# Performance work log

Hardware: AMD Instinct MI355X
Metric: run time of the kernel (lower is better)

The kernel has to match this reference:

```python
import jax, jax.numpy as jnp
import numpy as np

B, N_C, N_T = 8, 2048, 2048
D_S, D_F = 2, 1
K = 32
EMB_OBS = 4
H = 64
N_RBF = 16
NUM_BLKS = 6
RBF_GAMMA = 10.0


def _layer_norm(x, g, b):
    m = jnp.mean(x, -1, keepdims=True)
    v = jnp.var(x, -1, keepdims=True)
    return (x - m) * jax.lax.rsqrt(v + 1e-6) * g + b


def setup_inputs() -> dict:
    key = jax.random.key(0)
    ks = jax.random.split(key, 16)
    D_IN = EMB_OBS + D_S + D_F  # obs-flag embed + coords + features = 7
    return {
        "s_ctx": jax.random.normal(ks[0], (B, N_C, D_S)),
        "f_ctx": jax.random.normal(ks[1], (B, N_C, D_F)),
        "s_test": jax.random.normal(ks[2], (B, N_T, D_S)),
        "obs_table": jax.random.normal(ks[3], (2, EMB_OBS)) * 0.1,
        "emb_w0": jax.random.normal(ks[4], (D_IN, 256)) / np.sqrt(D_IN),
        "emb_b0": jnp.zeros((256,)),
        "emb_w1": jax.random.normal(ks[5], (256, 128)) / np.sqrt(256.0),
        "emb_b1": jnp.zeros((128,)),
        "emb_w2": jax.random.normal(ks[6], (128, H)) / np.sqrt(128.0),
        "emb_b2": jnp.zeros((H,)),
        "ln_g": jnp.ones((H,)),
        "ln_b": jnp.zeros((H,)),
        "rbf_centers": jnp.tile(jnp.linspace(0.0, 4.0, N_RBF)[None, :], (NUM_BLKS, 1)),
        "rbf_w": jax.random.normal(ks[7], (NUM_BLKS, N_RBF)) / np.sqrt(N_RBF),
        "rbf_b": jnp.zeros((NUM_BLKS,)),
        "blk_w1": jax.random.normal(ks[8], (NUM_BLKS, 2 * H, 2 * H)) / np.sqrt(2.0 * H),
        "blk_b1": jnp.zeros((NUM_BLKS, 2 * H)),
        "blk_w2": jax.random.normal(ks[9], (NUM_BLKS, 2 * H, H)) / np.sqrt(2.0 * H),
        "blk_b2": jnp.zeros((NUM_BLKS, H)),
        "blk_ln_g": jnp.ones((NUM_BLKS, H)),
        "blk_ln_b": jnp.zeros((NUM_BLKS, H)),
        "head_w0": jax.random.normal(ks[10], (H, 256)) / np.sqrt(float(H)),
        "head_b0": jnp.zeros((256,)),
        "head_w1": jax.random.normal(ks[11], (256, 64)) / np.sqrt(256.0),
        "head_b1": jnp.zeros((64,)),
        "head_w2": jax.random.normal(ks[12], (64, 2)) / np.sqrt(64.0),
        "head_b2": jnp.zeros((2,)),
    }


def reference(s_ctx, f_ctx, s_test, obs_table, emb_w0, emb_b0, emb_w1, emb_b1,
              emb_w2, emb_b2, ln_g, ln_b, rbf_centers, rbf_w, rbf_b,
              blk_w1, blk_b1, blk_w2, blk_b2, blk_ln_g, blk_ln_b,
              head_w0, head_b0, head_w1, head_b1, head_w2, head_b2):
    Bq, N_c = s_ctx.shape[:2]
    N_t = s_test.shape[1]

    # --- embed: obs flag + coords + (zeroed for test) function values ---
    obs_c = jnp.broadcast_to(obs_table[1], (Bq, N_c, EMB_OBS))  # observed = 1
    obs_t = jnp.broadcast_to(obs_table[0], (Bq, N_t, EMB_OBS))  # unobserved = 0
    f_test = jnp.zeros((Bq, N_t, f_ctx.shape[-1]), f_ctx.dtype)
    ctx = jnp.concatenate([obs_c, s_ctx, f_ctx], -1)
    test = jnp.concatenate([obs_t, s_test, f_test], -1)

    def emb(x):
        h = jax.nn.gelu(x @ emb_w0 + emb_b0)
        h = jax.nn.gelu(h @ emb_w1 + emb_b1)
        return h @ emb_w2 + emb_b2

    x_ctx = _layer_norm(emb(ctx), ln_g, ln_b)
    x_test = _layer_norm(emb(test), ln_g, ln_b)

    # --- kNN graph build (queries -> context senders) ---
    def knn(q, s):
        d2 = jnp.sum((q[:, :, None, :] - s[:, None, :, :]) ** 2, -1)  # (B, Nq, Nc)
        neg, idx = jax.lax.top_k(-d2, K)
        return idx, jnp.sqrt(jnp.maximum(-neg, 1e-12))

    idx_cc, d_cc = knn(s_ctx, s_ctx)
    idx_ct, d_ct = knn(s_test, s_ctx)
    off = (jnp.arange(Bq) * N_c)[:, None, None]
    senders = jnp.concatenate([(idx_cc + off).reshape(-1), (idx_ct + off).reshape(-1)])
    edges = jnp.concatenate([d_cc.reshape(-1), d_ct.reshape(-1)])
    nodes = jnp.concatenate([x_ctx.reshape(Bq * N_c, H), x_test.reshape(Bq * N_t, H)], 0)
    n_node = Bq * (N_c + N_t)
    # receivers = repeat(arange(n_node), K): each node owns a contiguous K-edge block
    send2d = senders.reshape(n_node, K)
    e2d = edges.reshape(n_node, K)
    mask2d = jnp.isfinite(e2d)
    e_safe = jnp.where(mask2d, e2d, 0.0)

    # --- RBF-biased message-passing blocks ---
    for l in range(NUM_BLKS):
        feats = jnp.exp(-RBF_GAMMA * (e_safe[..., None] - rbf_centers[l]) ** 2)  # (n_node, K, N_RBF)
        bias = feats @ rbf_w[l] + rbf_b[l]                                       # (n_node, K)
        bias = jnp.where(mask2d, bias, -1e9)
        w = jax.nn.softmax(bias, axis=-1)
        agg = jnp.einsum('nk,nkh->nh', w, nodes[send2d])  # gather senders + weighted sum
        h = jnp.concatenate([nodes, agg], -1)
        h = jax.nn.gelu(h @ blk_w1[l] + blk_b1[l])
        h = h @ blk_w2[l] + blk_b2[l]
        nodes = _layer_norm(nodes + h, blk_ln_g[l], blk_ln_b[l])

    # --- head + diagonal MVN ---
    x_t = nodes[-Bq * N_t:].reshape(Bq, N_t, H)
    h = jax.nn.gelu(x_t @ head_w0 + head_b0)
    h = jax.nn.gelu(h @ head_w1 + head_b1)
    out = h @ head_w2 + head_b2
    mean = out[..., 0]
    std = jax.nn.softplus(out[..., 1]) + 1e-3
    return mean, std
```

## Files before the change

kernel.cpp:

```cpp
#include <hip/hip_runtime.h>
#include <hip/hip_bf16.h>
#include <hip/hip_fp16.h>
#include <math.h>

using bf16 = __hip_bfloat16;

#define N_CTX   2048
#define N_TST   2048
#define NB      8
#define KNN     32
#define HDIM    64
#define NRBF    16
#define N_CTX_NODES (NB * N_CTX)
#define N_NODE      (NB * (N_CTX + N_TST))
#define POOL_CAP 256

typedef __attribute__((ext_vector_type(8))) short short8;
typedef __attribute__((ext_vector_type(4))) float f32x4;

#define SWZ(r, k) ((k) ^ (((r) & 7) << 3))

__device__ __forceinline__ bool is_f32(const void* probe) {
    return ((const unsigned short*)probe)[0] == 0;
}
template<bool F32>
__device__ __forceinline__ float ldT(const void* p, int i) {
    if constexpr (F32) return ((const float*)p)[i];
    else               return __bfloat162float(((const bf16*)p)[i]);
}
__device__ __forceinline__ float ld(const void* p, int i, bool f32) {
    return f32 ? ((const float*)p)[i]
               : __bfloat162float(((const bf16*)p)[i]);
}
__device__ __forceinline__ unsigned short f2b(float x) {
    bf16 h = __float2bfloat16(x); unsigned short u;
    __builtin_memcpy(&u, &h, 2); return u;
}
__device__ __forceinline__ float b2f(unsigned short u) {
    bf16 h; __builtin_memcpy(&h, &u, 2); return __bfloat162float(h);
}
__device__ __forceinline__ unsigned short f2h(float x) {
    __half h = __float2half(x); unsigned short u;
    __builtin_memcpy(&u, &h, 2); return u;
}
__device__ __forceinline__ float h2f(unsigned short u) {
    __half h; __builtin_memcpy(&h, &u, 2); return __half2float(h);
}
__device__ __forceinline__ float gelu_tanh(float x) {
    float u = -1.5957691216057308f * (x + 0.044715f * x * x * x);
    return x * __builtin_amdgcn_rcpf(1.0f + __expf(u));
}
__device__ __forceinline__ unsigned long long shfl_u64(unsigned long long v, int src) {
    int lo = __shfl((int)(unsigned)v, src);
    int hi = __shfl((int)(unsigned)(v >> 32), src);
    return ((unsigned long long)(unsigned)hi << 32) | (unsigned)lo;
}

__device__ __forceinline__ void batch_barrier(unsigned* cnt, unsigned target) {
    __syncthreads();
    if (threadIdx.x == 0) {
        __hip_atomic_fetch_add(cnt, 1u, __ATOMIC_RELEASE, __HIP_MEMORY_SCOPE_AGENT);
        unsigned v;
        do {
            v = __hip_atomic_load(cnt, __ATOMIC_ACQUIRE, __HIP_MEMORY_SCOPE_AGENT);
            if (v < target) __builtin_amdgcn_s_sleep(2);
        } while (v < target);
    }
    __syncthreads();
}

__global__ void prep_w_kernel(const void* w1, const void* w2, const void* probe,
                              unsigned short* __restrict__ w1t,
                              unsigned short* __restrict__ w2t) {
    bool f32 = is_f32(probe);
    int l = blockIdx.x >> 3, s = blockIdx.x & 7, t = threadIdx.x;
    for (int idx = s * 2048 + t; idx < (s + 1) * 2048; idx += 256) {
        int k = idx >> 7, c = idx & 127;
        w1t[l * 16384 + c * 128 + k] = f2b(ld(w1, l * 16384 + idx, f32));
    }
    for (int idx = s * 1024 + t; idx < (s + 1) * 1024; idx += 256) {
        int k = idx >> 6, c = idx & 63;
        w2t[l * 8192 + c * 128 + k] = f2b(ld(w2, l * 8192 + idx, f32));
    }
}

template<bool F32>
__device__ __forceinline__ void embed_body(
        const void* s_ctx, const void* f_ctx, const void* s_test, const void* obs,
        const void* w0, const void* b0, const void* w1, const void* b1,
        const void* w2, const void* b2, const void* ln_g, const void* ln_b,
        unsigned short* __restrict__ ctxb, float* __restrict__ testf,
        unsigned short* A, unsigned short* W, unsigned short* H0, unsigned short* W2) {
    int tid = threadIdx.x, w = tid >> 6, l = tid & 63;
    int nb = blockIdx.x * 64;
    bool is_test = (nb >= N_CTX_NODES);
    int loc0 = is_test ? nb - N_CTX_NODES : nb;
    int b = loc0 >> 11;

    for (int idx = tid; idx < 64 * 128; idx += 512) A[idx] = 0;
    for (int idx = tid; idx < 256 * 128; idx += 512) W[idx] = 0;
    __syncthreads();

    {   int nn = tid >> 3, slot = tid & 7;
        if (slot < 7) {
            int loc = loc0 + nn;
            int i = loc & (N_CTX - 1);
            float v;
            if (slot < 4)       v = ldT<F32>(obs, (is_test ? 0 : 1) * 4 + slot);
            else if (slot < 6)  v = is_test ? ldT<F32>(s_test, (b * N_TST + i) * 2 + slot - 4)
                                            : ldT<F32>(s_ctx,  (b * N_CTX + i) * 2 + slot - 4);
            else                v = is_test ? 0.0f : ldT<F32>(f_ctx, b * N_CTX + i);
            A[nn * 128 + SWZ(nn, slot)] = f2b(v);
        }
    }
    for (int idx = tid; idx < 7 * 256; idx += 512) {
        int k = idx >> 8, c = idx & 255;
        W[c * 128 + SWZ(c, k)] = f2b(ldT<F32>(w0, idx));
    }
    __syncthreads();

    {
        int rt = w & 3, co = w >> 2;
        int ra = rt * 16 + (l & 15);
        int kb = (l >> 4) << 3;
        short8 av = *(const short8*)&A[ra * 128 + SWZ(ra, kb)];
        f32x4 acc[8];
        #pragma unroll
        for (int c8 = 0; c8 < 8; ++c8) acc[c8] = (f32x4){0.f, 0.f, 0.f, 0.f};
        #pragma unroll
        for (int c8 = 0; c8 < 8; ++c8) {
            int cb = co * 8 + c8;
            int rb = cb * 16 + (l & 15);
            short8 bv = *(const short8*)&W[rb * 128 + SWZ(rb, kb)];
            acc[c8] = __builtin_amdgcn_mfma_f32_16x16x32_bf16(av, bv, acc[c8], 0, 0, 0);
        }
        #pragma unroll
        for (int c8 = 0; c8 < 8; ++c8) {
            int col = (co * 8 + c8) * 16 + (l & 15);
            float bb = ldT<F32>(b0, col);
            #pragma unroll
            for (int reg = 0; reg < 4; ++reg) {
                int r = rt * 16 + (l >> 4) * 4 + reg;
                H0[r * 256 + SWZ(r, col)] = f2b(gelu_tanh(acc[c8][reg] + bb));
            }
        }
    }
    __syncthreads();

    for (int idx = tid; idx < 256 * 128; idx += 512) {
        int k = idx >> 7, c = idx & 127;
        W[c * 256 + SWZ(c, k)] = f2b(ldT<F32>(w1, idx));
    }
    for (int idx = tid; idx < 128 * 64; idx += 512) {
        int k = idx >> 6, c = idx & 63;
        W2[c * 128 + SWZ(c, k)] = f2b(ldT<F32>(w2, idx));
    }
    __syncthreads();

    {
        int rt = w & 3, cq = w >> 2;
        int ra = rt * 16 + (l & 15);
        f32x4 acc[4];
        #pragma unroll
        for (int c4 = 0; c4 < 4; ++c4) acc[c4] = (f32x4){0.f, 0.f, 0.f, 0.f};
        #pragma unroll
        for (int ks = 0; ks < 8; ++ks) {
            int kb = ks * 32 + ((l >> 4) << 3);
            short8 av = *(const short8*)&H0[ra * 256 + SWZ(ra, kb)];
            #pragma unroll
            for (int c4 = 0; c4 < 4; ++c4) {
                int cb = cq * 4 + c4;
                int rb = cb * 16 + (l & 15);
                short8 bv = *(const short8*)&W[rb * 256 + SWZ(rb, kb)];
                acc[c4] = __builtin_amdgcn_mfma_f32_16x16x32_bf16(av, bv, acc[c4], 0, 0, 0);
            }
        }
        #pragma unroll
        for (int c4 = 0; c4 < 4; ++c4) {
            int col = (cq * 4 + c4) * 16 + (l & 15);
            float bb = ldT<F32>(b1, col);
            #pragma unroll
            for (int reg = 0; reg < 4; ++reg) {
                int r = rt * 16 + (l >> 4) * 4 + reg;
                A[r * 128 + SWZ(r, col)] = f2b(gelu_tanh(acc[c4][reg] + bb));
            }
        }
    }
    __syncthreads();

    if (w < 4) {
        f32x4 a2[4];
        #pragma unroll
        for (int cb = 0; cb < 4; ++cb) a2[cb] = (f32x4){0.f, 0.f, 0.f, 0.f};
        int ra = w * 16 + (l & 15);
        #pragma unroll
        for (int ks = 0; ks < 4; ++ks) {
            int kb = ks * 32 + ((l >> 4) << 3);
            short8 av = *(const short8*)&A[ra * 128 + SWZ(ra, kb)];
            #pragma unroll
            for (int cb = 0; cb < 4; ++cb) {
                int rb = cb * 16 + (l & 15);
                short8 bv = *(const short8*)&W2[rb * 128 + SWZ(rb, kb)];
                a2[cb] = __builtin_amdgcn_mfma_f32_16x16x32_bf16(av, bv, a2[cb], 0, 0, 0);
            }
        }
        int colb = l & 15;
        float g4[4], bb4[4], b24[4];
        #pragma unroll
        for (int cb = 0; cb < 4; ++cb) {
            int col = cb * 16 + colb;
            g4[cb]  = ldT<F32>(ln_g, col);
            bb4[cb] = ldT<F32>(ln_b, col);
            b24[cb] = ldT<F32>(b2,  col);
        }
        #pragma unroll
        for (int reg = 0; reg < 4; ++reg) {
            int r = w * 16 + (l >> 4) * 4 + reg;
            float vv[4]; float s = 0.f, s2 = 0.f;
            #pragma unroll
            for (int cb = 0; cb < 4; ++cb) {
                float v = a2[cb][reg] + b24[cb];
                vv[cb] = v; s += v; s2 += v * v;
            }
            #pragma unroll
            for (int o = 8; o > 0; o >>= 1) { s += __shfl_xor(s, o); s2 += __shfl_xor(s2, o); }
            float m = s / 64.0f;
            float var = s2 / 64.0f - m * m;
            float rs = rsqrtf(var + 1e-6f);
            #pragma unroll
            for (int cb = 0; cb < 4; ++cb) {
                int col = cb * 16 + colb;
                float val = (vv[cb] - m) * rs * g4[cb] + bb4[cb];
                if (is_test) testf[(loc0 + r) * HDIM + col] = val;
                else         ctxb[(size_t)(nb + r) * HDIM + col] = f2b(val);
            }
        }
    }
}

__global__ __launch_bounds__(512)
void embed_kernel(const void* s_ctx, const void* f_ctx, const void* s_test,
                  const void* obs, const void* w0, const void* b0,
                  const void* w1, const void* b1, const void* w2, const void* b2,
                  const void* ln_g, const void* ln_b,
                  unsigned short* __restrict__ ctxb, float* __restrict__ testf) {
    __shared__ unsigned short A[64 * 128];
    __shared__ unsigned short W[256 * 128];
    __shared__ unsigned short H0[64 * 256];
    __shared__ unsigned short W2[64 * 128];
    if (is_f32(ln_g))
        embed_body<true>(s_ctx, f_ctx, s_test, obs, w0, b0, w1, b1, w2, b2,
                         ln_g, ln_b, ctxb, testf, A, W, H0, W2);
    else
        embed_body<false>(s_ctx, f_ctx, s_test, obs, w0, b0, w1, b1, w2, b2,
                          ln_g, ln_b, ctxb, testf, A, W, H0, W2);
}

__global__ __launch_bounds__(512) void knn_kernel(const void* s_ctx, const void* s_test,
                                                  const void* probe,
                                                  unsigned short* __restrict__ knn_idx) {
    bool f32 = is_f32(probe);
    int w = threadIdx.x >> 6, l = threadIdx.x & 63;
    int n = blockIdx.x * 8 + w;
    __shared__ float cx[N_CTX], cy[N_CTX];
    __shared__ unsigned long long pool[8][POOL_CAP];
    __shared__ unsigned pcnt[8];

    bool is_test = (n >= N_CTX_NODES);
    int loc = is_test ? n - N_CTX_NODES : n;
    int b = loc >> 11, q = loc & (N_CTX - 1);

    for (int j = threadIdx.x; j < N_CTX; j += 512) {
        cx[j] = ld(s_ctx, (b * N_CTX + j) * 2 + 0, f32);
        cy[j] = ld(s_ctx, (b * N_CTX + j) * 2 + 1, f32);
    }
    __syncthreads();

    float qx = is_test ? ld(s_test, (b * N_TST + q) * 2 + 0, f32) : cx[q];
    float qy = is_test ? ld(s_test, (b * N_TST + q) * 2 + 1, f32) : cy[q];

    unsigned dbits[32];
    unsigned bmin = 0xFFFFFFFFu;
    #pragma unroll
    for (int i = 0; i < 32; ++i) {
        int j = i * 64 + l;
        float dx = qx - cx[j], dy = qy - cy[j];
        float d2 = __fadd_rn(__fmul_rn(dx, dx), __fmul_rn(dy, dy));
        unsigned ub = __float_as_uint(d2);
        dbits[i] = ub;
        bmin = min(bmin, ub);
    }

    unsigned T = 0;
    #pragma unroll
    for (int bit = 31; bit >= 0; --bit) {
        unsigned trial = T | (1u << bit);
        int c = __popcll(__ballot(bmin < trial));
        if (c < 32) T = trial;
    }

    if (l == 0) pcnt[w] = 0;
    unsigned mycnt = 0;
    #pragma unroll
    for (int i = 0; i < 32; ++i) mycnt += (dbits[i] <= T) ? 1u : 0u;
    unsigned off = atomicAdd(&pcnt[w], mycnt);
    #pragma unroll
    for (int i = 0; i < 32; ++i) {
        if (dbits[i] <= T) {
            if (off < POOL_CAP)
                pool[w][off] = ((unsigned long long)dbits[i] << 32) | (unsigned)(i * 64 + l);
            ++off;
        }
    }
    asm volatile("s_waitcnt lgkmcnt(0)" ::: "memory");
    unsigned M = pcnt[w];
    if (M > POOL_CAP) M = POOL_CAP;

    if (M <= 128) {
        unsigned long long my0 = (l < (int)M) ? pool[w][l] : ~0ull;
        unsigned long long my1 = (64 + l < (int)M) ? pool[w][64 + l] : ~0ull;
        unsigned r0 = 0, r1 = 0;
        unsigned M0 = M < 64 ? M : 64;
        for (unsigned jp = 0; jp < M0; ++jp) {
            unsigned long long v = shfl_u64(my0, (int)jp);
            r0 += (v < my0) ? 1u : 0u;
            r1 += (v < my1) ? 1u : 0u;
        }
        for (unsigned jp = 64; jp < M; ++jp) {
            unsigned long long v = shfl_u64(my1, (int)(jp - 64));
            r0 += (v < my0) ? 1u : 0u;
            r1 += (v < my1) ? 1u : 0u;
        }
        if (l < (int)M && r0 < KNN)
            knn_idx[(size_t)n * KNN + r0] = (unsigned short)(my0 & 0xFFFFu);
        if (64 + l < (int)M && r1 < KNN)
            knn_idx[(size_t)n * KNN + r1] = (unsigned short)(my1 & 0xFFFFu);
    } else {
        for (unsigned m = l; m < M; m += 64) {
            unsigned long long me = pool[w][m];
            unsigned rank = 0;
            for (unsigned jp = 0; jp < M; ++jp)
                rank += (pool[w][jp] < me) ? 1u : 0u;
            if (rank < KNN)
                knn_idx[(size_t)n * KNN + rank] = (unsigned short)(me & 0xFFFFu);
        }
    }
}

__global__ __launch_bounds__(1024, 4)
void mp_coop_kernel(unsigned short* __restrict__ ctxA, unsigned short* __restrict__ ctxB,
                    float* __restrict__ testf,
                    const unsigned short* __restrict__ kidx,
                    unsigned* __restrict__ bar,
                    const unsigned short* __restrict__ w1tg,
                    const unsigned short* __restrict__ w2tg,
                    const void* s_ctx, const void* s_test,
                    const void* rbf_c, const void* rbf_w, const void* rbf_b,
                    const void* b1, const void* b2,
                    const void* lng, const void* lnb) {
    bool f32 = is_f32(lng);
    int tid = threadIdx.x, w = tid >> 6, l = tid & 63;

    int batch = blockIdx.x & 7;
    int slot  = blockIdx.x >> 3;
    bool isctx = (slot < 16);
    int lslot = slot & 15;
    int seg0 = batch * N_CTX + lslot * 128;
    int n0   = (isctx ? 0 : N_CTX_NODES) + seg0;
    int bofs = batch * N_CTX;
    unsigned* cnt = bar + batch * 16;

    __shared__ float          state[128 * 64];
    __shared__ unsigned short A0[128 * 128];
    __shared__ unsigned short h1s[128 * 128];
    __shared__ unsigned short wk_l[128 * 32];
    __shared__ unsigned short kidx_l[128 * 32];
    __shared__ unsigned short d_l[128 * 32];

    for (int idx = tid; idx < 128 * 64; idx += 1024)
        state[idx] = isctx ? b2f(ctxA[n0 * 64 + idx]) : testf[seg0 * 64 + idx];

    for (int idx = tid; idx < 4096; idx += 1024) {
        int i = idx >> 5, kk = idx & 31;
        int n = n0 + i;
        int q = lslot * 128 + i;
        float qx = isctx ? ld(s_ctx, (bofs + q) * 2 + 0, f32)
                         : ld(s_test, (batch * N_TST + q) * 2 + 0, f32);
        float qy = isctx ? ld(s_ctx, (bofs + q) * 2 + 1, f32)
                         : ld(s_test, (batch * N_TST + q) * 2 + 1, f32);
        int si = (int)kidx[(size_t)n * KNN + kk];
        kidx_l[idx] = (unsigned short)si;
        float dx = qx - ld(s_ctx, (bofs + si) * 2 + 0, f32);
        float dy = qy - ld(s_ctx, (bofs + si) * 2 + 1, f32);
        float d2 = __fadd_rn(__fmul_rn(dx, dx), __fmul_rn(dy, dy));
        d_l[idx] = f2h(sqrtf(fmaxf(d2, 1e-12f)));
    }
    __syncthreads();

    const unsigned short* cur = ctxA;
    unsigned short* nxt = ctxB;

    for (int layer = 0; layer < 6; ++layer) {
        for (int p = 0; p < 4; ++p) {
            int i = w * 8 + p * 2 + (l >> 5);
            int kk = l & 31;
            float d = h2f(d_l[i * 32 + kk]);
            float bias = ld(rbf_b, layer, f32);
            #pragma unroll
            for (int j = 0; j < NRBF; ++j) {
                float c = ld(rbf_c, layer * NRBF + j, f32);
                float u = d - c;
                bias += expf(-10.0f * u * u) * ld(rbf_w, layer * NRBF + j, f32);
            }
            float m = bias;
            #pragma unroll
            for (int o = 16; o > 0; o >>= 1) m = fmaxf(m, __shfl_xor(m, o));
            float e = expf(bias - m), s = e;
            #pragma unroll
            for (int o = 16; o > 0; o >>= 1) s += __shfl_xor(s, o);
            wk_l[i * 32 + kk] = f2h(e / s);
        }
        {
            int m = l & 31, h = l >> 5;
            for (int i = w * 8; i < w * 8 + 8; ++i) {
                A0[i * 128 + SWZ(i, l)] = f2b(state[i * 64 + l]);
                float a0 = 0.f, a1 = 0.f, c0 = 0.f, c1 = 0.f;
                #pragma unroll
                for (int k = 0; k < 16; k += 2) {
                    {
                        int kk = 2 * k + h;
                        int si = (int)kidx_l[i * 32 + kk];
                        unsigned u = *(const unsigned*)(cur + (size_t)(bofs + si) * 64 + 2 * m);
                        float wkv = h2f(wk_l[i * 32 + kk]);
                        a0 += wkv * __uint_as_float(u << 16);
                        a1 += wkv * __uint_as_float(u & 0xFFFF0000u);
                    }
                    {
                        int kk = 2 * (k + 1) + h;
                        int si = (int)kidx_l[i * 32 + kk];
                        unsigned u = *(const unsigned*)(cur + (size_t)(bofs + si) * 64 + 2 * m);
                        float wkv = h2f(wk_l[i * 32 + kk]);
                        c0 += wkv * __uint_as_float(u << 16);
                        c1 += wkv * __uint_as_float(u & 0xFFFF0000u);
                    }
                }
                a0 += c0; a1 += c1;
                a0 += __shfl_xor(a0, 32);
                a1 += __shfl_xor(a1, 32);
                if (h == 0) {
                    unsigned pk = (unsigned)f2b(a0) | ((unsigned)f2b(a1) << 16);
                    *(unsigned*)&A0[i * 128 + SWZ(i, 64 + 2 * m)] = pk;
                }
            }
        }
        __syncthreads();

        {
            const unsigned short* wB = w1tg + layer * 16384;
            f32x4 acc[4];
            #pragma unroll
            for (int c4 = 0; c4 < 4; ++c4) acc[c4] = (f32x4){0.f, 0.f, 0.f, 0.f};
            int ra = (w & 7) * 16 + (l & 15);
            #pragma unroll
            for (int ks = 0; ks < 4; ++ks) {
                int kb = ks * 32 + ((l >> 4) << 3);
                short8 av = *(const short8*)&A0[ra * 128 + SWZ(ra, kb)];
                #pragma unroll
                for (int c4 = 0; c4 < 4; ++c4) {
                    int cb = (w >> 3) * 4 + c4;
                    int rb = cb * 16 + (l & 15);
                    short8 bv = *(const short8*)&wB[rb * 128 + kb];
                    acc[c4] = __builtin_amdgcn_mfma_f32_16x16x32_bf16(av, bv, acc[c4], 0, 0, 0);
                }
            }
            #pragma unroll
            for (int c4 = 0; c4 < 4; ++c4) {
                int col = ((w >> 3) * 4 + c4) * 16 + (l & 15);
                float bb = ld(b1, layer * 128 + col, f32);
                #pragma unroll
                for (int reg = 0; reg < 4; ++reg) {
                    int r = (w & 7) * 16 + (l >> 4) * 4 + reg;
                    h1s[r * 128 + SWZ(r, col)] = f2b(gelu_tanh(acc[c4][reg] + bb));
                }
            }
        }
        __syncthreads();

        if (w < 8) {
            const unsigned short* wB2 = w2tg + layer * 8192;
            f32x4 a2[4];
            #pragma unroll
            for (int cb = 0; cb < 4; ++cb) a2[cb] = (f32x4){0.f, 0.f, 0.f, 0.f};
            int ra = w * 16 + (l & 15);
            #pragma unroll
            for (int ks = 0; ks < 4; ++ks) {
                int kb = ks * 32 + ((l >> 4) << 3);
                short8 av = *(const short8*)&h1s[ra * 128 + SWZ(ra, kb)];
                #pragma unroll
                for (int cb = 0; cb < 4; ++cb) {
                    int rb = cb * 16 + (l & 15);
                    short8 bv = *(const short8*)&wB2[rb * 128 + kb];
                    a2[cb] = __builtin_amdgcn_mfma_f32_16x16x32_bf16(av, bv, a2[cb], 0, 0, 0);
                }
            }
            int colb = l & 15;
            float g4[4], bb4[4], b24[4];
            #pragma unroll
            for (int cb = 0; cb < 4; ++cb) {
                int col = cb * 16 + colb;
                g4[cb]  = ld(lng, layer * 64 + col, f32);
                bb4[cb] = ld(lnb, layer * 64 + col, f32);
                b24[cb] = ld(b2,  layer * 64 + col, f32);
            }
            #pragma unroll
            for (int reg = 0; reg < 4; ++reg) {
                int r = w * 16 + (l >> 4) * 4 + reg;
                float vv[4]; float s = 0.f, s2 = 0.f;
                #pragma unroll
                for (int cb = 0; cb < 4; ++cb) {
                    int col = cb * 16 + colb;
                    float v = a2[cb][reg] + b24[cb] + state[r * 64 + col];
                    vv[cb] = v; s += v; s2 += v * v;
                }
                #pragma unroll
                for (int o = 8; o > 0; o >>= 1) { s += __shfl_xor(s, o); s2 += __shfl_xor(s2, o); }
                float m = s / 64.0f;
                float var = s2 / 64.0f - m * m;
                float rs = rsqrtf(var + 1e-6f);
                #pragma unroll
                for (int cb = 0; cb < 4; ++cb) {
                    int col = cb * 16 + colb;
                    state[r * 64 + col] = (vv[cb] - m) * rs * g4[cb] + bb4[cb];
                }
            }
        }
        __syncthreads();

        if (layer < 5) {
            if (isctx)
                for (int idx = tid; idx < 128 * 64; idx += 1024)
                    nxt[n0 * 64 + idx] = f2b(state[idx]);
            batch_barrier(cnt, 32u * (unsigned)(layer + 1));
            const unsigned short* t1 = cur; cur = nxt; nxt = (unsigned short*)t1;
        }
    }

    if (!isctx)
        for (int idx = tid; idx < 128 * 64; idx += 1024)
            testf[seg0 * 64 + idx] = state[idx];
}

template<bool F32>
__device__ __forceinline__ void head_body(
        const float* __restrict__ testf, const void* w0, const void* b0,
        const void* w1, const void* b1, const void* w2, const void* b2, void* out,
        float (*xs)[64], float (*h0)[256], float (*h1)[64]) {
    int t = threadIdx.x;
    int pb = blockIdx.x * 16;

    for (int idx = t; idx < 1024; idx += 256)
        xs[idx >> 6][idx & 63] = testf[(pb + (idx >> 6)) * HDIM + (idx & 63)];
    __syncthreads();

    {
        float bb = ldT<F32>(b0, t);
        float a[16];
        #pragma unroll
        for (int j = 0; j < 16; ++j) a[j] = bb;
        for (int i = 0; i < 64; ++i) {
            float wv = ldT<F32>(w0, i * 256 + t);
            #pragma unroll
            for (int j = 0; j < 16; ++j) a[j] += xs[j][i] * wv;
        }
        #pragma unroll
        for (int j = 0; j < 16; ++j) h0[j][t] = gelu_tanh(a[j]);
    }
    __syncthreads();

    {
        int c = t & 63, g = t >> 6;
        float bb = ldT<F32>(b1, c);
        float a0 = bb, a1 = bb, a2 = bb, a3 = bb;
        for (int i = 0; i < 256; ++i) {
            float wv = ldT<F32>(w1, i * 64 + c);
            a0 += h0[g][i] * wv;      a1 += h0[g + 4][i] * wv;
            a2 += h0[g + 8][i] * wv;  a3 += h0[g + 12][i] * wv;
        }
        h1[g][c]      = gelu_tanh(a0); h1[g + 4][c]  = gelu_tanh(a1);
        h1[g + 8][c]  = gelu_tanh(a2); h1[g + 12][c] = gelu_tanh(a3);
    }
    __syncthreads();

    if (t < 32) {
        int nn = t >> 1, j = t & 1;
        float a = ldT<F32>(b2, j);
        for (int i = 0; i < 64; ++i) a += h1[nn][i] * ldT<F32>(w2, i * 2 + j);
        float r;
        if (j == 0) r = a;
        else        r = fmaxf(a, 0.0f) + log1pf(expf(-fabsf(a))) + 1e-3f;
        int oi = j * 16384 + pb + nn;
        if constexpr (F32) ((float*)out)[oi] = r;
        else               ((bf16*)out)[oi]  = __float2bfloat16(r);
    }
}

__global__ void head_kernel(const float* __restrict__ testf,
                            const void* w0, const void* b0, const void* w1, const void* b1,
                            const void* w2, const void* b2, const void* probe, void* out) {
    __shared__ float xs[16][64];
    __shared__ float h0[16][256];
    __shared__ float h1[16][64];
    if (is_f32(probe)) head_body<true>(testf, w0, b0, w1, b1, w2, b2, out, xs, h0, h1);
    else               head_body<false>(testf, w0, b0, w1, b1, w2, b2, out, xs, h0, h1);
}

extern "C" void kernel_launch(void* const* d_in, const int* in_sizes, int n_in,
                              void* d_out, int out_size, void* d_ws, size_t ws_size,
                              hipStream_t stream) {
    void* s_ctx   = d_in[0];
    void* f_ctx   = d_in[1];
    void* s_test  = d_in[2];
    void* obs     = d_in[3];
    void* emb_w0  = d_in[4];
    void* emb_b0  = d_in[5];
    void* emb_w1  = d_in[6];
    void* emb_b1  = d_in[7];
    void* emb_w2  = d_in[8];
    void* emb_b2  = d_in[9];
    void* ln_g    = d_in[10];
    void* ln_b    = d_in[11];
    void* rbf_c   = d_in[12];
    void* rbf_w   = d_in[13];
    void* rbf_b   = d_in[14];
    void* blk_w1  = d_in[15];
    void* blk_b1  = d_in[16];
    void* blk_w2  = d_in[17];
    void* blk_b2  = d_in[18];
    void* blk_lng = d_in[19];
    void* blk_lnb = d_in[20];
    void* head_w0 = d_in[21];
    void* head_b0 = d_in[22];
    void* head_w1 = d_in[23];
    void* head_b1 = d_in[24];
    void* head_w2 = d_in[25];
    void* head_b2 = d_in[26];

    unsigned short* ctxA  = (unsigned short*)d_ws;
    unsigned short* ctxB  = (unsigned short*)((char*)d_ws + 2097152);
    float*          testf = (float*)((char*)d_ws + 4194304);
    unsigned short* kidx  = (unsigned short*)((char*)d_ws + 8388608);
    unsigned*       bar   = (unsigned*)((char*)d_ws + 10485760);
    unsigned short* w1t   = (unsigned short*)((char*)d_ws + 10486272);
    unsigned short* w2t   = (unsigned short*)((char*)d_ws + 10682880);

    hipMemsetAsync(bar, 0, 8 * 16 * sizeof(unsigned), stream);

    prep_w_kernel<<<48, 256, 0, stream>>>(blk_w1, blk_w2, ln_g, w1t, w2t);

    embed_kernel<<<N_NODE / 64, 512, 0, stream>>>(s_ctx, f_ctx, s_test, obs,
        emb_w0, emb_b0, emb_w1, emb_b1, emb_w2, emb_b2, ln_g, ln_b, ctxA, testf);

    knn_kernel<<<N_NODE / 8, 512, 0, stream>>>(s_ctx, s_test, ln_g, kidx);

    void* kargs[] = { &ctxA, &ctxB, &testf, &kidx, &bar, &w1t, &w2t, &s_ctx, &s_test,
                      &rbf_c, &rbf_w, &rbf_b,
                      &blk_b1, &blk_b2, &blk_lng, &blk_lnb };
    hipLaunchCooperativeKernel((void*)mp_coop_kernel, dim3(256), dim3(1024),
                               kargs, 0, stream);

    head_kernel<<<16384 / 16, 256, 0, stream>>>(testf,
        head_w0, head_b0, head_w1, head_b1, head_w2, head_b2, ln_g, d_out);
}
```

Measured before the change: 412.8 us.

## Split message-passing cooperative kernel into smaller 64-node blocks

Adds a variant of the cooperative message-passing kernel in which each block handles 64 nodes with 512 threads, giving 512 blocks instead of 256 blocks of 1024 threads. The host queries occupancy and uses the small variant when at least two such blocks fit per CU, otherwise it falls back to the original. The aim is to spread work over more CUs and raise occupancy, at the cost of twice as many participants in each per-batch barrier and half as many MFMA waves in the second GEMM. Index arithmetic is also widened to size_t.

Measured after the change: 410.2 us. No clear change (-0.6%).

```diff
diff --git a/kernel.cpp b/kernel.cpp
--- a/kernel.cpp
+++ b/kernel.cpp
@@ -347,43 +347,43 @@
     }
 }
 
-__global__ __launch_bounds__(1024, 4)
-void mp_coop_kernel(unsigned short* __restrict__ ctxA, unsigned short* __restrict__ ctxB,
-                    float* __restrict__ testf,
-                    const unsigned short* __restrict__ kidx,
-                    unsigned* __restrict__ bar,
-                    const unsigned short* __restrict__ w1tg,
-                    const unsigned short* __restrict__ w2tg,
-                    const void* s_ctx, const void* s_test,
-                    const void* rbf_c, const void* rbf_w, const void* rbf_b,
-                    const void* b1, const void* b2,
-                    const void* lng, const void* lnb) {
+__global__ __launch_bounds__(512, 4)
+void mp_small_kernel(unsigned short* __restrict__ ctxA, unsigned short* __restrict__ ctxB,
+                     float* __restrict__ testf,
+                     const unsigned short* __restrict__ kidx,
+                     unsigned* __restrict__ bar,
+                     const unsigned short* __restrict__ w1tg,
+                     const unsigned short* __restrict__ w2tg,
+                     const void* s_ctx, const void* s_test,
+                     const void* rbf_c, const void* rbf_w, const void* rbf_b,
+                     const void* b1, const void* b2,
+                     const void* lng, const void* lnb) {
     bool f32 = is_f32(lng);
     int tid = threadIdx.x, w = tid >> 6, l = tid & 63;
 
     int batch = blockIdx.x & 7;
     int slot  = blockIdx.x >> 3;
-    bool isctx = (slot < 16);
-    int lslot = slot & 15;
-    int seg0 = batch * N_CTX + lslot * 128;
+    bool isctx = (slot < 32);
+    int lslot = slot & 31;
+    int seg0 = batch * N_CTX + lslot * 64;
     int n0   = (isctx ? 0 : N_CTX_NODES) + seg0;
     int bofs = batch * N_CTX;
     unsigned* cnt = bar + batch * 16;
 
-    __shared__ float          state[128 * 64];
-    __shared__ unsigned short A0[128 * 128];
-    __shared__ unsigned short h1s[128 * 128];
-    __shared__ unsigned short wk_l[128 * 32];
-    __shared__ unsigned short kidx_l[128 * 32];
-    __shared__ unsigned short d_l[128 * 32];
-
-    for (int idx = tid; idx < 128 * 64; idx += 1024)
-        state[idx] = isctx ? b2f(ctxA[n0 * 64 + idx]) : testf[seg0 * 64 + idx];
-
-    for (int idx = tid; idx < 4096; idx += 1024) {
+    __shared__ float          state[64 * 64];
+    __shared__ unsigned short A0[64 * 128];
+    __shared__ unsigned short h1s[64 * 128];
+    __shared__ unsigned short wk_l[64 * 32];
+    __shared__ unsigned short kidx_l[64 * 32];
+    __shared__ unsigned short d_l[64 * 32];
+
+    for (int idx = tid; idx < 64 * 64; idx += 512)
+        state[idx] = isctx ? b2f(ctxA[(size_t)n0 * 64 + idx]) : testf[(size_t)seg0 * 64 + idx];
+
+    for (int idx = tid; idx < 2048; idx += 512) {
         int i = idx >> 5, kk = idx & 31;
         int n = n0 + i;
-        int q = lslot * 128 + i;
+        int q = lslot * 64 + i;
         float qx = isctx ? ld(s_ctx, (bofs + q) * 2 + 0, f32)
                          : ld(s_test, (batch * N_TST + q) * 2 + 0, f32);
         float qy = isctx ? ld(s_ctx, (bofs + q) * 2 + 1, f32)
@@ -460,6 +460,209 @@
             f32x4 acc[4];
             #pragma unroll
             for (int c4 = 0; c4 < 4; ++c4) acc[c4] = (f32x4){0.f, 0.f, 0.f, 0.f};
+            int ra = (w & 3) * 16 + (l & 15);
+            #pragma unroll
+            for (int ks = 0; ks < 4; ++ks) {
+                int kb = ks * 32 + ((l >> 4) << 3);
+                short8 av = *(const short8*)&A0[ra * 128 + SWZ(ra, kb)];
+                #pragma unroll
+                for (int c4 = 0; c4 < 4; ++c4) {
+                    int cb = (w >> 2) * 4 + c4;
+                    int rb = cb * 16 + (l & 15);
+                    short8 bv = *(const short8*)&wB[rb * 128 + kb];
+                    acc[c4] = __builtin_amdgcn_mfma_f32_16x16x32_bf16(av, bv, acc[c4], 0, 0, 0);
+                }
+            }
+            #pragma unroll
+            for (int c4 = 0; c4 < 4; ++c4) {
+                int col = ((w >> 2) * 4 + c4) * 16 + (l & 15);
+                float bb = ld(b1, layer * 128 + col, f32);
+                #pragma unroll
+                for (int reg = 0; reg < 4; ++reg) {
+                    int r = (w & 3) * 16 + (l >> 4) * 4 + reg;
+                    h1s[r * 128 + SWZ(r, col)] = f2b(gelu_tanh(acc[c4][reg] + bb));
+                }
+            }
+        }
+        __syncthreads();
+
+        if (w < 4) {
+            const unsigned short* wB2 = w2tg + layer * 8192;
+            f32x4 a2[4];
+            #pragma unroll
+            for (int cb = 0; cb < 4; ++cb) a2[cb] = (f32x4){0.f, 0.f, 0.f, 0.f};
+            int ra = w * 16 + (l & 15);
+            #pragma unroll
+            for (int ks = 0; ks < 4; ++ks) {
+                int kb = ks * 32 + ((l >> 4) << 3);
+                short8 av = *(const short8*)&h1s[ra * 128 + SWZ(ra, kb)];
+                #pragma unroll
+                for (int cb = 0; cb < 4; ++cb) {
+                    int rb = cb * 16 + (l & 15);
+                    short8 bv = *(const short8*)&wB2[rb * 128 + kb];
+                    a2[cb] = __builtin_amdgcn_mfma_f32_16x16x32_bf16(av, bv, a2[cb], 0, 0, 0);
+                }
+            }
+            int colb = l & 15;
+            float g4[4], bb4[4], b24[4];
+            #pragma unroll
+            for (int cb = 0; cb < 4; ++cb) {
+                int col = cb * 16 + colb;
+                g4[cb]  = ld(lng, layer * 64 + col, f32);
+                bb4[cb] = ld(lnb, layer * 64 + col, f32);
+                b24[cb] = ld(b2,  layer * 64 + col, f32);
+            }
+            #pragma unroll
+            for (int reg = 0; reg < 4; ++reg) {
+                int r = w * 16 + (l >> 4) * 4 + reg;
+                float vv[4]; float s = 0.f, s2 = 0.f;
+                #pragma unroll
+                for (int cb = 0; cb < 4; ++cb) {
+                    int col = cb * 16 + colb;
+                    float v = a2[cb][reg] + b24[cb] + state[r * 64 + col];
+                    vv[cb] = v; s += v; s2 += v * v;
+                }
+                #pragma unroll
+                for (int o = 8; o > 0; o >>= 1) { s += __shfl_xor(s, o); s2 += __shfl_xor(s2, o); }
+                float m = s / 64.0f;
+                float var = s2 / 64.0f - m * m;
+                float rs = rsqrtf(var + 1e-6f);
+                #pragma unroll
+                for (int cb = 0; cb < 4; ++cb) {
+                    int col = cb * 16 + colb;
+                    state[r * 64 + col] = (vv[cb] - m) * rs * g4[cb] + bb4[cb];
+                }
+            }
+        }
+        __syncthreads();
+
+        if (layer < 5) {
+            if (isctx)
+                for (int idx = tid; idx < 4096; idx += 512)
+                    nxt[(size_t)n0 * 64 + idx] = f2b(state[idx]);
+            batch_barrier(cnt, 64u * (unsigned)(layer + 1));
+            const unsigned short* t1 = cur; cur = nxt; nxt = (unsigned short*)t1;
+        }
+    }
+
+    if (!isctx)
+        for (int idx = tid; idx < 4096; idx += 512)
+            testf[(size_t)seg0 * 64 + idx] = state[idx];
+}
+
+__global__ __launch_bounds__(1024, 4)
+void mp_coop_kernel(unsigned short* __restrict__ ctxA, unsigned short* __restrict__ ctxB,
+                    float* __restrict__ testf,
+                    const unsigned short* __restrict__ kidx,
+                    unsigned* __restrict__ bar,
+                    const unsigned short* __restrict__ w1tg,
+                    const unsigned short* __restrict__ w2tg,
+                    const void* s_ctx, const void* s_test,
+                    const void* rbf_c, const void* rbf_w, const void* rbf_b,
+                    const void* b1, const void* b2,
+                    const void* lng, const void* lnb) {
+    bool f32 = is_f32(lng);
+    int tid = threadIdx.x, w = tid >> 6, l = tid & 63;
+
+    int batch = blockIdx.x & 7;
+    int slot  = blockIdx.x >> 3;
+    bool isctx = (slot < 16);
+    int lslot = slot & 15;
+    int seg0 = batch * N_CTX + lslot * 128;
+    int n0   = (isctx ? 0 : N_CTX_NODES) + seg0;
+    int bofs = batch * N_CTX;
+    unsigned* cnt = bar + batch * 16;
+
+    __shared__ float          state[128 * 64];
+    __shared__ unsigned short A0[128 * 128];
+    __shared__ unsigned short h1s[128 * 128];
+    __shared__ unsigned short wk_l[128 * 32];
+    __shared__ unsigned short kidx_l[128 * 32];
+    __shared__ unsigned short d_l[128 * 32];
+
+    for (int idx = tid; idx < 128 * 64; idx += 1024)
+        state[idx] = isctx ? b2f(ctxA[(size_t)n0 * 64 + idx]) : testf[(size_t)seg0 * 64 + idx];
+
+    for (int idx = tid; idx < 4096; idx += 1024) {
+        int i = idx >> 5, kk = idx & 31;
+        int n = n0 + i;
+        int q = lslot * 128 + i;
+        float qx = isctx ? ld(s_ctx, (bofs + q) * 2 + 0, f32)
+                         : ld(s_test, (batch * N_TST + q) * 2 + 0, f32);
+        float qy = isctx ? ld(s_ctx, (bofs + q) * 2 + 1, f32)
+                         : ld(s_test, (batch * N_TST + q) * 2 + 1, f32);
+        int si = (int)kidx[(size_t)n * KNN + kk];
+        kidx_l[idx] = (unsigned short)si;
+        float dx = qx - ld(s_ctx, (bofs + si) * 2 + 0, f32);
+        float dy = qy - ld(s_ctx, (bofs + si) * 2 + 1, f32);
+        float d2 = __fadd_rn(__fmul_rn(dx, dx), __fmul_rn(dy, dy));
+        d_l[idx] = f2h(sqrtf(fmaxf(d2, 1e-12f)));
+    }
+    __syncthreads();
+
+    const unsigned short* cur = ctxA;
+    unsigned short* nxt = ctxB;
+
+    for (int layer = 0; layer < 6; ++layer) {
+        for (int p = 0; p < 4; ++p) {
+            int i = w * 8 + p * 2 + (l >> 5);
+            int kk = l & 31;
+            float d = h2f(d_l[i * 32 + kk]);
+            float bias = ld(rbf_b, layer, f32);
+            #pragma unroll
+            for (int j = 0; j < NRBF; ++j) {
+                float c = ld(rbf_c, layer * NRBF + j, f32);
+                float u = d - c;
+                bias += expf(-10.0f * u * u) * ld(rbf_w, layer * NRBF + j, f32);
+            }
+            float m = bias;
+            #pragma unroll
+            for (int o = 16; o > 0; o >>= 1) m = fmaxf(m, __shfl_xor(m, o));
+            float e = expf(bias - m), s = e;
+            #pragma unroll
+            for (int o = 16; o > 0; o >>= 1) s += __shfl_xor(s, o);
+            wk_l[i * 32 + kk] = f2h(e / s);
+        }
+        {
+            int m = l & 31, h = l >> 5;
+            for (int i = w * 8; i < w * 8 + 8; ++i) {
+                A0[i * 128 + SWZ(i, l)] = f2b(state[i * 64 + l]);
+                float a0 = 0.f, a1 = 0.f, c0 = 0.f, c1 = 0.f;
+                #pragma unroll
+                for (int k = 0; k < 16; k += 2) {
+                    {
+                        int kk = 2 * k + h;
+                        int si = (int)kidx_l[i * 32 + kk];
+                        unsigned u = *(const unsigned*)(cur + (size_t)(bofs + si) * 64 + 2 * m);
+                        float wkv = h2f(wk_l[i * 32 + kk]);
+                        a0 += wkv * __uint_as_float(u << 16);
+                        a1 += wkv * __uint_as_float(u & 0xFFFF0000u);
+                    }
+                    {
+                        int kk = 2 * (k + 1) + h;
+                        int si = (int)kidx_l[i * 32 + kk];
+                        unsigned u = *(const unsigned*)(cur + (size_t)(bofs + si) * 64 + 2 * m);
+                        float wkv = h2f(wk_l[i * 32 + kk]);
+                        c0 += wkv * __uint_as_float(u << 16);
+                        c1 += wkv * __uint_as_float(u & 0xFFFF0000u);
+                    }
+                }
+                a0 += c0; a1 += c1;
+                a0 += __shfl_xor(a0, 32);
+                a1 += __shfl_xor(a1, 32);
+                if (h == 0) {
+                    unsigned pk = (unsigned)f2b(a0) | ((unsigned)f2b(a1) << 16);
+                    *(unsigned*)&A0[i * 128 + SWZ(i, 64 + 2 * m)] = pk;
+                }
+            }
+        }
+        __syncthreads();
+
+        {
+            const unsigned short* wB = w1tg + layer * 16384;
+            f32x4 acc[4];
+            #pragma unroll
+            for (int c4 = 0; c4 < 4; ++c4) acc[c4] = (f32x4){0.f, 0.f, 0.f, 0.f};
             int ra = (w & 7) * 16 + (l & 15);
             #pragma unroll
             for (int ks = 0; ks < 4; ++ks) {
@@ -539,7 +742,7 @@
         if (layer < 5) {
             if (isctx)
                 for (int idx = tid; idx < 128 * 64; idx += 1024)
-                    nxt[n0 * 64 + idx] = f2b(state[idx]);
+                    nxt[(size_t)n0 * 64 + idx] = f2b(state[idx]);
             batch_barrier(cnt, 32u * (unsigned)(layer + 1));
             const unsigned short* t1 = cur; cur = nxt; nxt = (unsigned short*)t1;
         }
@@ -547,7 +750,7 @@
 
     if (!isctx)
         for (int idx = tid; idx < 128 * 64; idx += 1024)
-            testf[seg0 * 64 + idx] = state[idx];
+            testf[(size_t)seg0 * 64 + idx] = state[idx];
 }
 
 template<bool F32>
@@ -562,8 +765,7 @@
         xs[idx >> 6][idx & 63] = testf[(pb + (idx >> 6)) * HDIM + (idx & 63)];
     __syncthreads();
 
-    {
-        float bb = ldT<F32>(b0, t);
+    {   float bb = ldT<F32>(b0, t);
         float a[16];
         #pragma unroll
         for (int j = 0; j < 16; ++j) a[j] = bb;
@@ -577,8 +779,7 @@
     }
     __syncthreads();
 
-    {
-        int c = t & 63, g = t >> 6;
+    {   int c = t & 63, g = t >> 6;
         float bb = ldT<F32>(b1, c);
         float a0 = bb, a1 = bb, a2 = bb, a3 = bb;
         for (int i = 0; i < 256; ++i) {
@@ -665,8 +866,17 @@
     void* kargs[] = { &ctxA, &ctxB, &testf, &kidx, &bar, &w1t, &w2t, &s_ctx, &s_test,
                       &rbf_c, &rbf_w, &rbf_b,
                       &blk_b1, &blk_b2, &blk_lng, &blk_lnb };
-    hipLaunchCooperativeKernel((void*)mp_coop_kernel, dim3(256), dim3(1024),
-                               kargs, 0, stream);
+
+    int bpc = 0;
+    hipError_t qerr = hipOccupancyMaxActiveBlocksPerMultiprocessor(
+        &bpc, (const void*)mp_small_kernel, 512, 0);
+    if (qerr == hipSuccess && bpc >= 2) {
+        hipLaunchCooperativeKernel((void*)mp_small_kernel, dim3(512), dim3(512),
+                                   kargs, 0, stream);
+    } else {
+        hipLaunchCooperativeKernel((void*)mp_coop_kernel, dim3(256), dim3(1024),
+                                   kargs, 0, stream);
+    }
 
     head_kernel<<<16384 / 16, 256, 0, stream>>>(testf,
         head_w0, head_b0, head_w1, head_b1, head_w2, head_b2, ln_g, d_out);
```
